# Kernel optimization log

Hardware: AMD Instinct MI355X
Metric: run time of the kernel (lower is better)

The kernel has to match this reference:

```python
import jax, jax.numpy as jnp
import numpy as np
import itertools

B, K, H, W = 64, 5, 320, 320
EPS = 1e-6
# All K! permutations (exact equivalent of scipy.linear_sum_assignment for KxK cost)
PERMS = np.array(list(itertools.permutations(range(K))), dtype=np.int32)  # [P, K]


def setup_inputs() -> dict:
    key = jax.random.key(0)
    k1, k2, k3 = jax.random.split(key, 3)
    return {
        "fg_logits": jax.random.normal(k1, (B, 1, H, W), dtype=jnp.float32),
        "slot_logits": jax.random.normal(k2, (B, K, H, W), dtype=jnp.float32),
        "target": jax.random.uniform(k3, (B, 1, H, W), dtype=jnp.float32),
    }


def reference(fg_logits, slot_logits, target):
    fg = target[:, 0]            # [B,H,W]
    bg = 1.0 - fg                # [B,H,W]
    # targets_b: index 0 = FG mask, 1..K-1 = BG mask (duplicated)  -> [B,K,H,W]
    targets = jnp.concatenate([fg[:, None], jnp.broadcast_to(bg[:, None], (B, K - 1, H, W))], axis=1)

    # IoU cost matrix on detached sigmoid probs (matches .detach())
    probs = jax.lax.stop_gradient(jax.nn.sigmoid(slot_logits))
    s = probs.reshape(B, K, -1)        # [B,K,N]
    t = targets.reshape(B, K, -1)      # [B,K,N]
    inter = jnp.einsum('bkn,bjn->bkj', s, t)           # [B,K,K]
    union = s.sum(-1)[:, :, None] + t.sum(-1)[:, None, :] - inter + EPS
    cost = 1.0 - inter / union                          # [B,K,K]

    # Exact Hungarian via brute force over K! permutations (K small)
    perms = jnp.asarray(PERMS)                          # [P,K]
    rows = jnp.arange(K)[None, :]                       # [1,K]
    perm_cost = cost[:, rows, perms].sum(-1)            # [B,P]
    best_perm = perms[jnp.argmin(perm_cost, axis=1)]    # [B,K] col_ind per sample

    # aligned[i] = targets[col_ind[i]]; targets[j] is fg iff j == 0
    is_fg = (best_perm == 0)[:, :, None, None]          # [B,K,1,1]
    aligned = jnp.where(is_fg, fg[:, None], bg[:, None])  # [B,K,H,W]

    # Stable sigmoid-BCE with logits, mean-reduced per sample then averaged over B
    x = slot_logits
    bce = jnp.maximum(x, 0.0) - x * aligned + jnp.log1p(jnp.exp(-jnp.abs(x)))
    return bce.mean()
```

## Files before the change

### kernel.cpp

```cpp
#include <hip/hip_runtime.h>


#define BB 64
#define KK 5
#define NPIX 102400
#define CHUNKS 25
#define CHUNK_PIX 4096
#define THREADS 256
#define NV 21
#define STRIDE 24

__global__ __launch_bounds__(THREADS) void hung_pass1(
    const float* __restrict__ slot,
    const float* __restrict__ tgt,
    float* __restrict__ ws)
{
    const int b  = blockIdx.y;
    const int cx = blockIdx.x;
    const float* t  = tgt  + (size_t)b * NPIX;
    const float* xb = slot + (size_t)b * KK * NPIX;

    float A[KK] = {0,0,0,0,0};
    float C[KK] = {0,0,0,0,0};
    float I[KK] = {0,0,0,0,0};
    float S[KK] = {0,0,0,0,0};
    float Tf = 0.0f;

    const int base = cx * CHUNK_PIX;
    #pragma unroll
    for (int it = 0; it < CHUNK_PIX / (THREADS * 4); ++it) {
        const int pix = base + it * (THREADS * 4) + threadIdx.x * 4;
        const float4 fg4 = *reinterpret_cast<const float4*>(t + pix);
        Tf += (fg4.x + fg4.y) + (fg4.z + fg4.w);
        float fgv[4] = {fg4.x, fg4.y, fg4.z, fg4.w};
        #pragma unroll
        for (int k = 0; k < KK; ++k) {
            const float4 x4 = *reinterpret_cast<const float4*>(xb + (size_t)k * NPIX + pix);
            float xv[4] = {x4.x, x4.y, x4.z, x4.w};
            #pragma unroll
            for (int j = 0; j < 4; ++j) {
                const float x  = xv[j];
                const float fg = fgv[j];
                const float e   = __expf(-fabsf(x));
                const float inv = __builtin_amdgcn_rcpf(1.0f + e);
                const float s   = (x >= 0.0f) ? inv : e * inv;
                const float sp  = fmaxf(x, 0.0f) + __logf(1.0f + e);
                A[k] += sp - x * (1.0f - fg);
                C[k] += x * (2.0f * fg - 1.0f);
                I[k] += s * fg;
                S[k] += s;
            }
        }
    }

    float vals[NV];
    #pragma unroll
    for (int k = 0; k < KK; ++k) {
        vals[k]      = A[k];
        vals[5 + k]  = C[k];
        vals[10 + k] = I[k];
        vals[15 + k] = S[k];
    }
    vals[20] = Tf;

    #pragma unroll
    for (int j = 0; j < NV; ++j) {
        float v = vals[j];
        #pragma unroll
        for (int off = 32; off > 0; off >>= 1) v += __shfl_down(v, off, 64);
        vals[j] = v;
    }
    __shared__ float red[THREADS / 64][NV];
    const int lane = threadIdx.x & 63;
    const int wv   = threadIdx.x >> 6;
    if (lane == 0) {
        #pragma unroll
        for (int j = 0; j < NV; ++j) red[wv][j] = vals[j];
    }
    __syncthreads();
    if (threadIdx.x < NV) {
        const float sum = red[0][threadIdx.x] + red[1][threadIdx.x]
                        + red[2][threadIdx.x] + red[3][threadIdx.x];
        ws[((size_t)(cx * BB + b)) * STRIDE + threadIdx.x] = sum;
    }
}

__global__ __launch_bounds__(64) void hung_pass2(
    const float* __restrict__ ws, float* __restrict__ out)
{
    const int b = threadIdx.x;
    float v[NV];
    #pragma unroll
    for (int j = 0; j < NV; ++j) v[j] = 0.0f;
    for (int c = 0; c < CHUNKS; ++c) {
        const float* p = ws + ((size_t)(c * BB + b)) * STRIDE;
        #pragma unroll
        for (int j = 0; j < NV; ++j) v[j] += p[j];
    }
    const float Tf = v[20];
    const float Tb = (float)NPIX - Tf;
    float best = 3.402823466e+38f;
    int   kb   = 0;
    float sumA = 0.0f;
    #pragma unroll
    for (int k = 0; k < KK; ++k) {
        const float Iv = v[10 + k], Sv = v[15 + k];
        const float cf = 1.0f - Iv / (Sv + Tf - Iv + 1e-6f);
        const float Ib = Sv - Iv;
        const float cb = 1.0f - Ib / (Sv + Tb - Ib + 1e-6f);
        const float d  = cf - cb;
        if (d < best) { best = d; kb = k; }
        sumA += v[k];
    }
    float tot = sumA - v[5 + kb];
    #pragma unroll
    for (int off = 32; off > 0; off >>= 1) tot += __shfl_down(tot, off, 64);
    if (b == 0) out[0] = tot * (1.0f / ((float)BB * (float)KK * (float)NPIX));
}

extern "C" void kernel_launch(void* const* d_in, const int* in_sizes, int n_in,
                              void* d_out, int out_size, void* d_ws, size_t ws_size,
                              hipStream_t stream) {
    const float* slot = (const float*)d_in[1];
    const float* tgt  = (const float*)d_in[2];
    float* out = (float*)d_out;
    float* ws  = (float*)d_ws;

    dim3 grid(CHUNKS, BB);
    hung_pass1<<<grid, THREADS, 0, stream>>>(slot, tgt, ws);
    hung_pass2<<<1, 64, 0, stream>>>(ws, out);
}
```

Baseline: 256.0 us.

## Reformulate BCE sums, halve chunk size, and reduce partials via global atomics

Rewrites the per-pixel math so that sigmoid comes from exp(-(softplus - x)) and the accumulators become x, x*fg, s and s*fg, with a single shared softplus-minus-x sum. This drops the reciprocal and select. Chunks shrink to 2048 pixels, giving twice as many blocks, and occupancy is hinted via launch bounds. Per-wave results are atomically added into one per-sample record, which replaces the shared-memory reduce and the per-chunk workspace; the workspace is zeroed by an extra kernel launch. Atomic float accumulation makes the result order-nondeterministic and adds contention on 22 addresses per sample.

```diff
diff --git a/kernel.cpp b/kernel.cpp
--- a/kernel.cpp
+++ b/kernel.cpp
@@ -4,13 +4,16 @@
 #define BB 64
 #define KK 5
 #define NPIX 102400
-#define CHUNKS 25
-#define CHUNK_PIX 4096
+#define CHUNK_PIX 2048
+#define CHUNKS 50
 #define THREADS 256
-#define NV 21
-#define STRIDE 24
+#define REC 32
 
-__global__ __launch_bounds__(THREADS) void hung_pass1(
+__global__ __launch_bounds__(1024) void hung_zero(float* __restrict__ ws) {
+    ws[blockIdx.x * 1024 + threadIdx.x] = 0.0f;
+}
+
+__global__ __launch_bounds__(THREADS, 4) void hung_pass1(
     const float* __restrict__ slot,
     const float* __restrict__ tgt,
     float* __restrict__ ws)
@@ -20,68 +23,67 @@
     const float* t  = tgt  + (size_t)b * NPIX;
     const float* xb = slot + (size_t)b * KK * NPIX;
 
-    float A[KK] = {0,0,0,0,0};
-    float C[KK] = {0,0,0,0,0};
-    float I[KK] = {0,0,0,0,0};
-    float S[KK] = {0,0,0,0,0};
-    float Tf = 0.0f;
+    float X[KK]  = {0,0,0,0,0};
+    float XF[KK] = {0,0,0,0,0};
+    float S[KK]  = {0,0,0,0,0};
+    float SF[KK] = {0,0,0,0,0};
+    float PX = 0.0f, Tf = 0.0f;
 
-    const int base = cx * CHUNK_PIX;
+    const int base = cx * CHUNK_PIX + threadIdx.x * 4;
     #pragma unroll
-    for (int it = 0; it < CHUNK_PIX / (THREADS * 4); ++it) {
-        const int pix = base + it * (THREADS * 4) + threadIdx.x * 4;
+    for (int h = 0; h < 2; ++h) {
+        const int pix = base + h * (THREADS * 4);
         const float4 fg4 = *reinterpret_cast<const float4*>(t + pix);
+        float4 x4[KK];
+        #pragma unroll
+        for (int k = 0; k < KK; ++k)
+            x4[k] = *reinterpret_cast<const float4*>(xb + (size_t)k * NPIX + pix);
+
         Tf += (fg4.x + fg4.y) + (fg4.z + fg4.w);
-        float fgv[4] = {fg4.x, fg4.y, fg4.z, fg4.w};
+        const float fgv[4] = {fg4.x, fg4.y, fg4.z, fg4.w};
         #pragma unroll
         for (int k = 0; k < KK; ++k) {
-            const float4 x4 = *reinterpret_cast<const float4*>(xb + (size_t)k * NPIX + pix);
-            float xv[4] = {x4.x, x4.y, x4.z, x4.w};
+            const float xv[4] = {x4[k].x, x4[k].y, x4[k].z, x4[k].w};
             #pragma unroll
             for (int j = 0; j < 4; ++j) {
                 const float x  = xv[j];
                 const float fg = fgv[j];
-                const float e   = __expf(-fabsf(x));
-                const float inv = __builtin_amdgcn_rcpf(1.0f + e);
-                const float s   = (x >= 0.0f) ? inv : e * inv;
-                const float sp  = fmaxf(x, 0.0f) + __logf(1.0f + e);
-                A[k] += sp - x * (1.0f - fg);
-                C[k] += x * (2.0f * fg - 1.0f);
-                I[k] += s * fg;
-                S[k] += s;
+                const float e  = __expf(-fabsf(x));
+                const float lg = __logf(1.0f + e);
+                const float sp = fmaxf(x, 0.0f) + lg;
+                const float d  = sp - x;
+                const float s  = __expf(-d);
+                PX    += d;
+                X[k]  += x;
+                XF[k]  = fmaf(x, fg, XF[k]);
+                S[k]  += s;
+                SF[k]  = fmaf(s, fg, SF[k]);
             }
         }
     }
 
-    float vals[NV];
+    float vals[22];
     #pragma unroll
     for (int k = 0; k < KK; ++k) {
-        vals[k]      = A[k];
-        vals[5 + k]  = C[k];
-        vals[10 + k] = I[k];
-        vals[15 + k] = S[k];
+        vals[k]      = X[k];
+        vals[5 + k]  = XF[k];
+        vals[10 + k] = S[k];
+        vals[15 + k] = SF[k];
     }
-    vals[20] = Tf;
+    vals[20] = PX;
+    vals[21] = Tf;
 
     #pragma unroll
-    for (int j = 0; j < NV; ++j) {
+    for (int j = 0; j < 22; ++j) {
         float v = vals[j];
         #pragma unroll
         for (int off = 32; off > 0; off >>= 1) v += __shfl_down(v, off, 64);
         vals[j] = v;
     }
-    __shared__ float red[THREADS / 64][NV];
-    const int lane = threadIdx.x & 63;
-    const int wv   = threadIdx.x >> 6;
-    if (lane == 0) {
+    if ((threadIdx.x & 63) == 0) {
+        float* rec = ws + (size_t)b * REC;
         #pragma unroll
-        for (int j = 0; j < NV; ++j) red[wv][j] = vals[j];
-    }
-    __syncthreads();
-    if (threadIdx.x < NV) {
-        const float sum = red[0][threadIdx.x] + red[1][threadIdx.x]
-                        + red[2][threadIdx.x] + red[3][threadIdx.x];
-        ws[((size_t)(cx * BB + b)) * STRIDE + threadIdx.x] = sum;
+        for (int j = 0; j < 22; ++j) unsafeAtomicAdd(rec + j, vals[j]);
     }
 }
 
@@ -89,33 +91,32 @@
     const float* __restrict__ ws, float* __restrict__ out)
 {
     const int b = threadIdx.x;
-    float v[NV];
-    #pragma unroll
-    for (int j = 0; j < NV; ++j) v[j] = 0.0f;
-    for (int c = 0; c < CHUNKS; ++c) {
-        const float* p = ws + ((size_t)(c * BB + b)) * STRIDE;
-        #pragma unroll
-        for (int j = 0; j < NV; ++j) v[j] += p[j];
-    }
-    const float Tf = v[20];
+    const float* v = ws + (size_t)b * REC;
+    const float PX = v[20];
+    const float Tf = v[21];
     const float Tb = (float)NPIX - Tf;
+
     float best = 3.402823466e+38f;
     int   kb   = 0;
-    float sumA = 0.0f;
+    float xfsum = 0.0f;
     #pragma unroll
     for (int k = 0; k < KK; ++k) {
-        const float Iv = v[10 + k], Sv = v[15 + k];
+        const float Iv = v[15 + k];
+        const float Sv = v[10 + k];
         const float cf = 1.0f - Iv / (Sv + Tf - Iv + 1e-6f);
         const float Ib = Sv - Iv;
         const float cb = 1.0f - Ib / (Sv + Tb - Ib + 1e-6f);
         const float d  = cf - cb;
         if (d < best) { best = d; kb = k; }
-        sumA += v[k];
+        xfsum += v[5 + k];
     }
-    float tot = sumA - v[5 + kb];
+    const float Ck  = 2.0f * v[5 + kb] - v[kb];
+    float res = PX + xfsum - Ck;
+
     #pragma unroll
-    for (int off = 32; off > 0; off >>= 1) tot += __shfl_down(tot, off, 64);
-    if (b == 0) out[0] = tot * (1.0f / ((float)BB * (float)KK * (float)NPIX));
+    for (int off = 32; off > 0; off >>= 1) res += __shfl_down(res, off, 64);
+    if (b == 0)
+        out[0] = res * (1.0f / ((float)BB * (float)KK * (float)NPIX));
 }
 
 extern "C" void kernel_launch(void* const* d_in, const int* in_sizes, int n_in,
@@ -126,6 +127,7 @@
     float* out = (float*)d_out;
     float* ws  = (float*)d_ws;
 
+    hung_zero<<<2, 1024, 0, stream>>>(ws);
     dim3 grid(CHUNKS, BB);
     hung_pass1<<<grid, THREADS, 0, stream>>>(slot, tgt, ws);
     hung_pass2<<<1, 64, 0, stream>>>(ws, out);
```

Measured after the change: 333.2 us. 1.3x slower.
